# Performance work log

Measured on AMD Instinct MI355X. Metric: run time of the kernel, lower is better.

The kernel has to match this reference:

```python
import jax, jax.numpy as jnp
import numpy as np

B, H, L, N, F = 32, 256, 2048, 64, 32  # batch, d_model, seq len, d_state//2 complex modes, num_features


def setup_inputs() -> dict:
    key = jax.random.key(0)
    ks = jax.random.split(key, 16)
    inp = {
        "x": jax.random.normal(ks[0], (B, H, L), jnp.float32),
        "t": jax.random.normal(ks[1], (B, H), jnp.float32),
        "features": jax.random.normal(ks[2], (B, F, L), jnp.float32),
        # time_linear
        "Wt": jax.random.normal(ks[3], (H, H), jnp.float32) / np.sqrt(H),
        "bt": jnp.zeros((H,), jnp.float32),
        # LayerNorm over d_model
        "ln_g": jnp.ones((H,), jnp.float32),
        "ln_b": jnp.zeros((H,), jnp.float32),
        # S4 (diagonal / S4D parameterization, d_state=128 -> N=64 complex, bidirectional)
        "log_dt": jnp.log(jnp.full((H,), 0.01, jnp.float32))
                  + jax.random.uniform(ks[4], (H,), jnp.float32, -1.0, 1.0),
        "logA_real": jnp.log(0.5 * jnp.ones((H, N), jnp.float32)),
        "A_imag": jnp.broadcast_to(np.pi * jnp.arange(N, dtype=jnp.float32), (H, N)).copy(),
        "C_re": jax.random.normal(ks[5], (2, H, N), jnp.float32) / np.sqrt(2 * N),
        "C_im": jax.random.normal(ks[6], (2, H, N), jnp.float32) / np.sqrt(2 * N),
        "D": jax.random.normal(ks[7], (H,), jnp.float32),
        # S4 output position-wise linear
        "Wout": jax.random.normal(ks[8], (H, H), jnp.float32) / np.sqrt(H),
        "bout": jnp.zeros((H,), jnp.float32),
        # out_linear1 / out_linear2 (1x1 convs)
        "W1": jax.random.normal(ks[9], (H, H), jnp.float32) / np.sqrt(H),
        "b1": jnp.zeros((H,), jnp.float32),
        "W2": jax.random.normal(ks[10], (H, H), jnp.float32) / np.sqrt(H),
        "b2": jnp.zeros((H,), jnp.float32),
        # feature_encoder 1x1 conv
        "Wf": jax.random.normal(ks[11], (H, F), jnp.float32) / np.sqrt(F),
        "bf": jnp.zeros((H,), jnp.float32),
    }
    return inp


def _s4_block(x, t, features, Wt, bt, ln_g, ln_b, log_dt, logA_real, A_imag,
              C_re, C_im, D, Wout, bout, W1, b1, W2, b2, Wf, bf):
    Bb, Hh, Ll = x.shape
    # time conditioning: Linear(t) broadcast over length  -> (B,H,L)
    tb = t @ Wt.T + bt
    xin = x + tb[:, :, None]
    # LayerNorm over channel (d_model) axis (norm applied on transposed tensor)
    mu = jnp.mean(xin, axis=1, keepdims=True)
    var = jnp.var(xin, axis=1, keepdims=True)
    z = (xin - mu) / jnp.sqrt(var + 1e-5) * ln_g[None, :, None] + ln_b[None, :, None]
    # --- bidirectional S4 (diagonal SSM) kernel ---
    dt = jnp.exp(log_dt)                       # (H,)
    A = -jnp.exp(logA_real) + 1j * A_imag      # (H,N)
    dtA = dt[:, None] * A                      # (H,N)
    Cd = (C_re + 1j * C_im) * (jnp.exp(dtA) - 1.0) / A      # (2,H,N) discretized C
    vand = jnp.exp(dtA[:, :, None] * jnp.arange(Ll))         # (H,N,L) Vandermonde
    K = 2.0 * jnp.real(jnp.einsum('chn,hnl->chl', Cd, vand))  # (2,H,L)
    zeros = jnp.zeros_like(K[0])
    k = jnp.concatenate([K[0], zeros], -1) + jnp.concatenate([zeros, K[1][:, ::-1]], -1)  # (H,2L)
    # FFT global convolution
    y = jnp.fft.irfft(jnp.fft.rfft(z, 2 * Ll) * jnp.fft.rfft(k, 2 * Ll)[None], 2 * Ll)[..., :Ll]
    y = y + z * D[None, :, None]
    y = jax.nn.gelu(y)
    y = jnp.einsum('bhl,gh->bgl', y, Wout) + bout[None, :, None]
    xr = y + xin                                # residual inside S4Layer
    # feature encoder + gated activation
    out = xr + jnp.einsum('bfl,hf->bhl', features, Wf) + bf[None, :, None]
    g = jnp.tanh(out) * jax.nn.sigmoid(out)
    o1 = jnp.einsum('bhl,gh->bgl', g, W1) + b1[None, :, None]
    o2 = jnp.einsum('bhl,gh->bgl', g, W2) + b2[None, :, None]
    return (o1 + x, o2)


def reference(x, t, features, Wt, bt, ln_g, ln_b, log_dt, logA_real, A_imag,
              C_re, C_im, D, Wout, bout, W1, b1, W2, b2, Wf, bf):
    return _s4_block(x, t, features, Wt, bt, ln_g, ln_b, log_dt, logA_real, A_imag,
                     C_re, C_im, D, Wout, bout, W1, b1, W2, b2, Wf, bf)
```

## Files before the change

### kernel.cpp

```cpp
#include <hip/hip_runtime.h>

typedef unsigned short ushort_t;

#define Bb 32
#define Hh 256
#define Ll 2048
#define Nn 64
#define BHL 16777216

typedef __bf16 bf16x8 __attribute__((ext_vector_type(8)));
typedef float f32x4 __attribute__((ext_vector_type(4)));
typedef unsigned int uint4v __attribute__((ext_vector_type(4)));

__device__ __forceinline__ ushort_t f2bf(float f) {
    unsigned int u = __float_as_uint(f);
    unsigned int r = ((u >> 16) & 1u) + 0x7fffu;
    return (ushort_t)((u + r) >> 16);
}
__device__ __forceinline__ float bf2f(ushort_t h) {
    return __uint_as_float(((unsigned int)h) << 16);
}
__device__ __forceinline__ float gelu_tanh(float v) {
    float u = 0.7978845608028654f * fmaf(0.044715f * v, v * v, v);
    float e = __expf(2.f * u);
    float th = 1.f - 2.f / (e + 1.f);
    return 0.5f * v * (1.f + th);
}
__device__ __forceinline__ float gate_fn(float v) {
    float sg = 1.f / (1.f + __expf(-v));
    float e2 = __expf(2.f * v);
    float th = 1.f - 2.f / (e2 + 1.f);
    return th * sg;
}
__device__ __forceinline__ uint4v rev8v(uint4v a) {
    union { uint4v v; ushort_t s8[8]; } x, y;
    x.v = a;
    #pragma unroll
    for (int j = 0; j < 8; ++j) y.s8[j] = x.s8[7 - j];
    return y.v;
}

__global__ __launch_bounds__(256) void prep_kernel(
    const float* __restrict__ t, const float* __restrict__ Wt, const float* __restrict__ bt,
    const float* __restrict__ Wout, const float* __restrict__ Wf,
    const float* __restrict__ bout, const float* __restrict__ bfb,
    const float* __restrict__ W1, const float* __restrict__ b1,
    const float* __restrict__ W2, const float* __restrict__ b2,
    float* __restrict__ tb, float* __restrict__ bc, float* __restrict__ b12,
    ushort_t* __restrict__ wcf, ushort_t* __restrict__ w12f)
{
    int bx = blockIdx.x, tid = threadIdx.x;
    __shared__ float trow[256];
    if (bx < 32) {
        trow[tid] = t[bx * 256 + tid];
        __syncthreads();
        float acc = bt[tid];
        #pragma unroll 4
        for (int hh = 0; hh < 256; ++hh) acc = fmaf(trow[hh], Wt[tid * 256 + hh], acc);
        tb[bx * 256 + tid] = acc;
    } else if (bx < 64) {
        int gt = (bx - 32) * 256 + tid;
        if (gt < 256) bc[gt] = bout[gt] + bfb[gt];
        if (gt < 512) b12[gt] = (gt < 256) ? b1[gt] : b2[gt - 256];
        for (int fg = gt; fg < 9216; fg += 8192) {
            int mt = fg / 576, rem = fg % 576;
            int kc = rem >> 6, lane = rem & 63;
            int m = mt * 16 + (lane & 15);
            int kb = kc * 32 + (lane >> 4) * 8;
            #pragma unroll
            for (int j = 0; j < 8; ++j) {
                int k = kb + j;
                float v = (k < 256) ? Wout[m * 256 + k] : Wf[m * 32 + (k - 256)];
                wcf[(size_t)fg * 8 + j] = f2bf(v);
            }
        }
    } else {
        int gt = (bx - 64) * 256 + tid;
        for (int fg = gt; fg < 16384; fg += 8192) {
            int mt = fg >> 9, rem = fg & 511;
            int kc = rem >> 6, lane = rem & 63;
            int m = mt * 16 + (lane & 15);
            int kb = kc * 32 + (lane >> 4) * 8;
            #pragma unroll
            for (int j = 0; j < 8; ++j) {
                int k = kb + j;
                float v = (m < 256) ? W1[m * 256 + k] : W2[(m - 256) * 256 + k];
                w12f[(size_t)fg * 8 + j] = f2bf(v);
            }
        }
    }
}

__global__ __launch_bounds__(256) void prep2_kernel(
    const float* __restrict__ log_dt, const float* __restrict__ logA, const float* __restrict__ Aimg,
    const float* __restrict__ C_re, const float* __restrict__ C_im,
    float* __restrict__ drg, float* __restrict__ dig,
    ushort_t* __restrict__ Mfrag, ushort_t* __restrict__ Vfrag)
{
    int bx = blockIdx.x, tid = threadIdx.x;
    int h = bx >> 1, dir = bx & 1;
    __shared__ float drL[64], diL[64], crL[64], ciL[64];
    __shared__ float ktab[128];
    __shared__ ushort_t bndL[128 * 128];
    if (tid < 64) {
        int n = tid;
        int idx = h * 64 + n;
        float dt = __expf(log_dt[h]);
        float Ar = -__expf(logA[idx]);
        float Ai = Aimg[idx];
        float dr = dt * Ar, di = dt * Ai;
        float er = __expf(dr);
        float wr_ = er * __cosf(di), wi_ = er * __sinf(di);
        float nr = wr_ - 1.f, ni = wi_;
        float inv = 1.f / (Ar * Ar + Ai * Ai);
        float qr = (nr * Ar + ni * Ai) * inv;
        float qi = (ni * Ar - nr * Ai) * inv;
        float cr = C_re[dir * 16384 + idx], ci = C_im[dir * 16384 + idx];
        drL[n] = dr; diL[n] = di;
        crL[n] = 2.f * (cr * qr - ci * qi);
        ciL[n] = 2.f * (cr * qi + ci * qr);
        if (dir == 0) { drg[idx] = dr; dig[idx] = di; }
    }
    __syncthreads();
    if (tid < 128) {
        int i = tid;
        float e = (float)(i + 1 - dir);
        #pragma unroll 4
        for (int n = 0; n < 64; ++n) {
            float ex = __expf(e * drL[n]);
            float ph = e * diL[n];
            float pr = ex * __cosf(ph), pi = ex * __sinf(ph);
            bndL[i * 128 + n]      = f2bf(crL[n] * pr - ciL[n] * pi);
            bndL[i * 128 + 64 + n] = f2bf(-(crL[n] * pi + ciL[n] * pr));
        }
    } else {
        int d = tid - 128;
        float e = (float)d;
        float acc = 0.f;
        #pragma unroll 4
        for (int n = 0; n < 64; ++n) {
            float ex = __expf(e * drL[n]);
            float ph = e * diL[n];
            acc += crL[n] * (ex * __cosf(ph)) - ciL[n] * (ex * __sinf(ph));
        }
        ktab[d] = acc;
    }
    __syncthreads();
    size_t base = (size_t)bx << 15;
    for (int idx = tid; idx < 32768; idx += 256) {
        int j = idx & 7, lane = (idx >> 3) & 63, kc = (idx >> 9) & 7, mt = idx >> 12;
        int m = mt * 16 + (lane & 15);
        int k = kc * 32 + (lane >> 4) * 8 + j;
        float v;
        if (k < 128) {
            int d = m - k - dir;
            v = (d >= 0) ? ktab[d] : 0.f;
        } else {
            v = bf2f(bndL[m * 128 + (k - 128)]);
        }
        Mfrag[base + idx] = f2bf(v);
    }
    if (dir == 0) {
        size_t vbase = (size_t)h << 14;
        for (int idx = tid; idx < 16384; idx += 256) {
            int j = idx & 7, lane = (idx >> 3) & 63, kc = (idx >> 9) & 3, mt = idx >> 11;
            int s = mt * 16 + (lane & 15);
            int k = kc * 32 + (lane >> 4) * 8 + j;
            int n = s & 63;
            float e = (float)(127 - k);
            float ex = __expf(e * drL[n]);
            float ph = e * diL[n];
            float v = (s < 64) ? ex * __cosf(ph) : ex * __sinf(ph);
            Vfrag[vbase + idx] = f2bf(v);
        }
    }
}

__global__ __launch_bounds__(256) void ln_kernel(
    const float* __restrict__ x, const float* __restrict__ tb,
    const float* __restrict__ ln_g, const float* __restrict__ ln_b,
    ushort_t* __restrict__ zbf)
{
    int gid = blockIdx.x * 256 + threadIdx.x;
    int b = gid >> 11, l = gid & 2047;
    const float* xp = x + (size_t)b * (Hh * Ll) + l;
    const float* tbp = tb + b * 256;
    float sum = 0.f, ssq = 0.f;
    #pragma unroll 8
    for (int h = 0; h < 256; ++h) {
        float v = xp[(size_t)h * Ll] + tbp[h];
        sum += v; ssq = fmaf(v, v, ssq);
    }
    float mean = sum * (1.f / 256.f);
    float var = fmaf(ssq, 1.f / 256.f, -mean * mean);
    float rstd = rsqrtf(var + 1e-5f);
    ushort_t* zp = zbf + (size_t)b * (Hh * Ll) + l;
    #pragma unroll 8
    for (int h = 0; h < 256; ++h) {
        float v = xp[(size_t)h * Ll] + tbp[h];
        zp[(size_t)h * Ll] = f2bf((v - mean) * rstd * ln_g[h] + ln_b[h]);
    }
}

__global__ __launch_bounds__(256) void ssm_mega_kernel(
    const ushort_t* __restrict__ zbf,
    const float* __restrict__ drg, const float* __restrict__ dig, const float* __restrict__ Dv,
    const ushort_t* __restrict__ Mfrag, const ushort_t* __restrict__ Vfrag,
    ushort_t* __restrict__ ya)
{
    __shared__ ushort_t Zs[64 * 136];
    __shared__ ushort_t Ssf[64 * 136];
    __shared__ ushort_t Ssb[64 * 136];
    __shared__ float Qb[2 * 128 * 17];
    int tid = threadIdx.x, lane = tid & 63, w = tid >> 6;
    int q = lane >> 4, cl = lane & 15;
    int h = blockIdx.x, cb = blockIdx.y;
    int b0 = cb * 4;
    for (int i = tid; i < 1024; i += 256) {
        int bsub = i >> 8, t8 = (i & 255) * 8;
        const ushort_t* zrow = zbf + ((size_t)((b0 + bsub) * 256 + h) << 11);
        *(uint4v*)&Zs[(bsub * 16 + (t8 >> 7)) * 136 + (t8 & 127)] = *(const uint4v*)(zrow + t8);
    }
    float dr0 = drg[h * 64 + lane], di0 = dig[h * 64 + lane];
    float ex128 = __expf(128.f * dr0);
    float w128r = ex128 * __cosf(128.f * di0);
    float w128i = ex128 * __sinf(128.f * di0);
    float Dh = Dv[h];
    __syncthreads();
    const ushort_t* vbase = Vfrag + ((size_t)h << 14);
    const ushort_t* mbase0 = Mfrag + ((size_t)(h * 2) << 15);
    const ushort_t* mbase1 = Mfrag + ((size_t)(h * 2 + 1) << 15);
    for (int bsub = 0; bsub < 4; ++bsub) {
        f32x4 qa[2][2] = {};
        #pragma unroll
        for (int kc = 0; kc < 4; ++kc) {
            int kk = kc * 32 + q * 8;
            bf16x8 bz = __builtin_bit_cast(bf16x8,
                *(const uint4v*)&Zs[(bsub * 16 + cl) * 136 + kk]);
            bf16x8 bzr = __builtin_bit_cast(bf16x8, rev8v(
                *(const uint4v*)&Zs[(bsub * 16 + (15 - cl)) * 136 + (120 - kk)]));
            #pragma unroll
            for (int i = 0; i < 2; ++i) {
                int mt = w * 2 + i;
                bf16x8 af = __builtin_bit_cast(bf16x8,
                    *(const uint4v*)(vbase + (((mt * 4 + kc) * 64 + lane) << 3)));
                qa[0][i] = __builtin_amdgcn_mfma_f32_16x16x32_bf16(af, bz, qa[0][i], 0, 0, 0);
                qa[1][i] = __builtin_amdgcn_mfma_f32_16x16x32_bf16(af, bzr, qa[1][i], 0, 0, 0);
            }
        }
        __syncthreads();
        #pragma unroll
        for (int d = 0; d < 2; ++d)
            #pragma unroll
            for (int i = 0; i < 2; ++i) {
                int mt = w * 2 + i;
                #pragma unroll
                for (int r = 0; r < 4; ++r)
                    Qb[d * 2176 + (mt * 16 + q * 4 + r) * 17 + cl] = qa[d][i][r];
            }
        __syncthreads();
        if (w < 2) {
            ushort_t* S = (w == 0) ? Ssf : Ssb;
            const float* Qp = Qb + w * 2176;
            float sre = 0.f, sim = 0.f;
            for (int cc = 0; cc < 16; ++cc) {
                S[(bsub * 16 + cc) * 136 + lane] = f2bf(sre);
                S[(bsub * 16 + cc) * 136 + 64 + lane] = f2bf(sim);
                float qre = Qp[lane * 17 + cc];
                float qim = Qp[(64 + lane) * 17 + cc];
                float nre = fmaf(w128r, sre, fmaf(-w128i, sim, qre));
                float nim = fmaf(w128r, sim, fmaf(w128i, sre, qim));
                sre = nre; sim = nim;
            }
        }
        __syncthreads();
    }
    f32x4 accf[2][4] = {}, accb[2][4] = {};
    for (int kc = 0; kc < 8; ++kc) {
        int kk = (kc & 3) * 32 + q * 8;
        bf16x8 aff[2], afb[2];
        #pragma unroll
        for (int i = 0; i < 2; ++i) {
            int mt = w * 2 + i;
            aff[i] = __builtin_bit_cast(bf16x8, *(const uint4v*)(mbase0 + (((mt * 8 + kc) * 64 + lane) << 3)));
            afb[i] = __builtin_bit_cast(bf16x8, *(const uint4v*)(mbase1 + (((mt * 8 + kc) * 64 + lane) << 3)));
        }
        #pragma unroll
        for (int nt = 0; nt < 4; ++nt) {
            bf16x8 bff, bfb_;
            if (kc < 4) {
                bff  = __builtin_bit_cast(bf16x8, *(const uint4v*)&Zs[(nt * 16 + cl) * 136 + kk]);
                bfb_ = __builtin_bit_cast(bf16x8, rev8v(
                       *(const uint4v*)&Zs[(nt * 16 + (15 - cl)) * 136 + (120 - kk)]));
            } else {
                bff  = __builtin_bit_cast(bf16x8, *(const uint4v*)&Ssf[(nt * 16 + cl) * 136 + kk]);
                bfb_ = __builtin_bit_cast(bf16x8, *(const uint4v*)&Ssb[(nt * 16 + cl) * 136 + kk]);
            }
            #pragma unroll
            for (int i = 0; i < 2; ++i) {
                accf[i][nt] = __builtin_amdgcn_mfma_f32_16x16x32_bf16(aff[i], bff,  accf[i][nt], 0, 0, 0);
                accb[i][nt] = __builtin_amdgcn_mfma_f32_16x16x32_bf16(afb[i], bfb_, accb[i][nt], 0, 0, 0);
            }
        }
    }
    __syncthreads();
    ushort_t* Yf = Ssf;
    ushort_t* Yb = Ssb;
    #pragma unroll
    for (int i = 0; i < 2; ++i) {
        int mt = w * 2 + i;
        #pragma unroll
        for (int nt = 0; nt < 4; ++nt) {
            int col = nt * 16 + cl;
            #pragma unroll
            for (int r = 0; r < 4; ++r) {
                int m = mt * 16 + q * 4 + r;
                Yf[col * 136 + m] = f2bf(accf[i][nt][r]);
                Yb[col * 136 + m] = f2bf(accb[i][nt][r]);
            }
        }
    }
    __syncthreads();
    for (int u = tid; u < 1024; u += 256) {
        int col = u >> 4, i0 = (u & 15) * 8;
        int bsub = col >> 4, c = col & 15;
        int colb = bsub * 16 + (15 - c);
        union { uint4v v; ushort_t s8[8]; } uf, uz, ub, uo;
        uf.v = *(const uint4v*)&Yf[col * 136 + i0];
        uz.v = *(const uint4v*)&Zs[col * 136 + i0];
        ub.v = rev8v(*(const uint4v*)&Yb[colb * 136 + (120 - i0)]);
        #pragma unroll
        for (int j = 0; j < 8; ++j) {
            float v = bf2f(uf.s8[j]) + bf2f(ub.s8[j]) + Dh * bf2f(uz.s8[j]);
            uo.s8[j] = f2bf(gelu_tanh(v));
        }
        ushort_t* yrow = ya + ((size_t)((b0 + bsub) * 256 + h) << 11);
        *(uint4v*)(yrow + c * 128 + i0) = uo.v;
    }
}

__global__ __launch_bounds__(256, 4) void gemm1_kernel(
    const ushort_t* __restrict__ ya, const float* __restrict__ feat,
    const float* __restrict__ x, const float* __restrict__ tb,
    const float* __restrict__ bc, const ushort_t* __restrict__ wcf,
    ushort_t* __restrict__ g)
{
    __shared__ __align__(16) ushort_t XT[64 * 48];
    int tid = threadIdx.x;
    int w = tid >> 6, lane = tid & 63;
    int bx = blockIdx.x;
    int b = bx >> 5;
    int l0 = (bx & 31) << 6;
    f32x4 acc[4][4] = {};
    int kk = tid >> 3, ng = tid & 7;
    for (int kc = 0; kc < 9; ++kc) {
        int k = kc * 32 + kk;
        union { uint4v v; ushort_t s[8]; } u;
        if (k < 256) {
            u.v = *(const uint4v*)(ya + ((size_t)(b * 256 + k) << 11) + l0 + ng * 8);
        } else {
            const float* src = feat + (size_t)(b * 32 + (k - 256)) * Ll + l0 + ng * 8;
            #pragma unroll
            for (int j = 0; j < 8; ++j) u.s[j] = f2bf(src[j]);
        }
        #pragma unroll
        for (int j = 0; j < 8; ++j) XT[(ng * 8 + j) * 48 + kk] = u.s[j];
        __syncthreads();
        bf16x8 af[4], bfr[4];
        #pragma unroll
        for (int i = 0; i < 4; ++i) {
            const ushort_t* p = wcf + ((size_t)((w * 4 + i) * 9 + kc) * 64 + lane) * 8;
            af[i] = __builtin_bit_cast(bf16x8, *(const uint4v*)p);
        }
        #pragma unroll
        for (int nt = 0; nt < 4; ++nt) {
            const ushort_t* p = &XT[(nt * 16 + (lane & 15)) * 48 + (lane >> 4) * 8];
            bfr[nt] = __builtin_bit_cast(bf16x8, *(const uint4v*)p);
        }
        #pragma unroll
        for (int i = 0; i < 4; ++i)
            #pragma unroll
            for (int nt = 0; nt < 4; ++nt)
                acc[i][nt] = __builtin_amdgcn_mfma_f32_16x16x32_bf16(af[i], bfr[nt], acc[i][nt], 0, 0, 0);
        __syncthreads();
    }
    int q = lane >> 4, nl = lane & 15;
    #pragma unroll
    for (int i = 0; i < 4; ++i) {
        #pragma unroll
        for (int nt = 0; nt < 4; ++nt) {
            int n = l0 + nt * 16 + nl;
            #pragma unroll
            for (int r = 0; r < 4; ++r) {
                int m = (w * 4 + i) * 16 + q * 4 + r;
                size_t oi = (size_t)(b * 256 + m) * Ll + n;
                float v = acc[i][nt][r] + bc[m] + tb[b * 256 + m] + x[oi];
                g[oi] = f2bf(gate_fn(v));
            }
        }
    }
}

__global__ __launch_bounds__(256, 4) void gemm2_kernel(
    const ushort_t* __restrict__ g, const float* __restrict__ x,
    const float* __restrict__ b12, const ushort_t* __restrict__ w12f,
    float* __restrict__ out)
{
    __shared__ __align__(16) ushort_t XT[64 * 48];
    int tid = threadIdx.x;
    int w = tid >> 6, lane = tid & 63;
    int bx = blockIdx.x;
    int half = blockIdx.y;
    int b = bx >> 5;
    int l0 = (bx & 31) << 6;
    f32x4 acc[4][4] = {};
    int kk = tid >> 3, ng = tid & 7;
    for (int kc = 0; kc < 8; ++kc) {
        int k = kc * 32 + kk;
        union { uint4v v; ushort_t s[8]; } u;
        u.v = *(const uint4v*)(g + (size_t)(b * 256 + k) * Ll + l0 + ng * 8);
        #pragma unroll
        for (int j = 0; j < 8; ++j) XT[(ng * 8 + j) * 48 + kk] = u.s[j];
        __syncthreads();
        bf16x8 af[4], bfr[4];
        #pragma unroll
        for (int i = 0; i < 4; ++i) {
            int mtg = half * 16 + w * 4 + i;
            const ushort_t* p = w12f + ((size_t)(mtg * 8 + kc) * 64 + lane) * 8;
            af[i] = __builtin_bit_cast(bf16x8, *(const uint4v*)p);
        }
        #pragma unroll
        for (int nt = 0; nt < 4; ++nt) {
            const ushort_t* p = &XT[(nt * 16 + (lane & 15)) * 48 + (lane >> 4) * 8];
            bfr[nt] = __builtin_bit_cast(bf16x8, *(const uint4v*)p);
        }
        #pragma unroll
        for (int i = 0; i < 4; ++i)
            #pragma unroll
            for (int nt = 0; nt < 4; ++nt)
                acc[i][nt] = __builtin_amdgcn_mfma_f32_16x16x32_bf16(af[i], bfr[nt], acc[i][nt], 0, 0, 0);
        __syncthreads();
    }
    int q = lane >> 4, nl = lane & 15;
    #pragma unroll
    for (int i = 0; i < 4; ++i) {
        #pragma unroll
        for (int nt = 0; nt < 4; ++nt) {
            int n = l0 + nt * 16 + nl;
            #pragma unroll
            for (int r = 0; r < 4; ++r) {
                int m = (w * 4 + i) * 16 + q * 4 + r;
                size_t oi = (size_t)(b * 256 + m) * Ll + n;
                float v = acc[i][nt][r] + b12[half * 256 + m];
                if (half == 0) out[oi] = v + x[oi];
                else out[(size_t)BHL + oi] = v;
            }
        }
    }
}

extern "C" void kernel_launch(void* const* d_in, const int* in_sizes, int n_in,
                              void* d_out, int out_size, void* d_ws, size_t ws_size,
                              hipStream_t stream) {
    const float* x      = (const float*)d_in[0];
    const float* t      = (const float*)d_in[1];
    const float* feat   = (const float*)d_in[2];
    const float* Wt     = (const float*)d_in[3];
    const float* bt     = (const float*)d_in[4];
    const float* ln_g   = (const float*)d_in[5];
    const float* ln_b   = (const float*)d_in[6];
    const float* log_dt = (const float*)d_in[7];
    const float* logA   = (const float*)d_in[8];
    const float* Aimg   = (const float*)d_in[9];
    const float* C_re   = (const float*)d_in[10];
    const float* C_im   = (const float*)d_in[11];
    const float* Dv     = (const float*)d_in[12];
    const float* Wout   = (const float*)d_in[13];
    const float* bout   = (const float*)d_in[14];
    const float* W1     = (const float*)d_in[15];
    const float* b1     = (const float*)d_in[16];
    const float* W2     = (const float*)d_in[17];
    const float* b2     = (const float*)d_in[18];
    const float* Wf     = (const float*)d_in[19];
    const float* bfb    = (const float*)d_in[20];

    char* ob = (char*)d_out;
    ushort_t* zbf = (ushort_t*)ob;
    ushort_t* yab = (ushort_t*)(ob + 33554432);
    float*    out = (float*)d_out;

    char* ws = (char*)d_ws;
    ushort_t* Mfrag = (ushort_t*)ws;
    ushort_t* gbuf  = (ushort_t*)ws;
    ushort_t* Vfrag = (ushort_t*)(ws + 33554432);
    char* ws2 = ws + 33554432 + 8388608;
    float* tb   = (float*)ws2;
    float* drg  = (float*)(ws2 + 32768);
    float* dig  = (float*)(ws2 + 98304);
    float* bc   = (float*)(ws2 + 163840);
    float* b12  = (float*)(ws2 + 164864);
    ushort_t* wcf  = (ushort_t*)(ws2 + 166912);
    ushort_t* w12f = (ushort_t*)(ws2 + 314368);

    prep_kernel<<<96, 256, 0, stream>>>(t, Wt, bt, Wout, Wf, bout, bfb, W1, b1, W2, b2,
                                        tb, bc, b12, wcf, w12f);
    prep2_kernel<<<512, 256, 0, stream>>>(log_dt, logA, Aimg, C_re, C_im, drg, dig, Mfrag, Vfrag);
    ln_kernel<<<256, 256, 0, stream>>>(x, tb, ln_g, ln_b, zbf);
    ssm_mega_kernel<<<dim3(256, 8), 256, 0, stream>>>(zbf, drg, dig, Dv, Mfrag, Vfrag, yab);
    gemm1_kernel<<<1024, 256, 0, stream>>>(yab, feat, x, tb, bc, wcf, gbuf);
    gemm2_kernel<<<dim3(1024, 2), 256, 0, stream>>>(gbuf, x, b12, w12f, out);
}
```

Measured before the change: 428.5 us.

## Fuse gate GEMMs via LDS, merge prep kernels, tile LayerNorm through shared memory

The two output GEMMs become one kernel: the gated activation is written to an LDS tile and fed straight into the W1/W2 GEMM, so the bf16 intermediate no longer goes through global memory and there is one launch fewer. The two prep kernels are merged into a single launch. LayerNorm now stages a 256x64 slab of x in LDS with float4 loads and writes with 8-byte stores, instead of reading x twice with strided per-thread access. The fused GEMM holds twice as many accumulators and uses about 34KB of extra LDS, lowering occupancy, and the SSM output buffer moves from the output region into the workspace.

```diff
diff --git a/kernel.cpp b/kernel.cpp
--- a/kernel.cpp
+++ b/kernel.cpp
@@ -11,6 +11,7 @@
 typedef __bf16 bf16x8 __attribute__((ext_vector_type(8)));
 typedef float f32x4 __attribute__((ext_vector_type(4)));
 typedef unsigned int uint4v __attribute__((ext_vector_type(4)));
+typedef unsigned int uint2v __attribute__((ext_vector_type(2)));
 
 __device__ __forceinline__ ushort_t f2bf(float f) {
     unsigned int u = __float_as_uint(f);
@@ -40,17 +41,24 @@
     return y.v;
 }
 
-__global__ __launch_bounds__(256) void prep_kernel(
+__global__ __launch_bounds__(256) void prep_all_kernel(
     const float* __restrict__ t, const float* __restrict__ Wt, const float* __restrict__ bt,
     const float* __restrict__ Wout, const float* __restrict__ Wf,
     const float* __restrict__ bout, const float* __restrict__ bfb,
     const float* __restrict__ W1, const float* __restrict__ b1,
     const float* __restrict__ W2, const float* __restrict__ b2,
+    const float* __restrict__ log_dt, const float* __restrict__ logA, const float* __restrict__ Aimg,
+    const float* __restrict__ C_re, const float* __restrict__ C_im,
     float* __restrict__ tb, float* __restrict__ bc, float* __restrict__ b12,
-    ushort_t* __restrict__ wcf, ushort_t* __restrict__ w12f)
+    ushort_t* __restrict__ wcf, ushort_t* __restrict__ w12f,
+    float* __restrict__ drg, float* __restrict__ dig,
+    ushort_t* __restrict__ Mfrag, ushort_t* __restrict__ Vfrag)
 {
     int bx = blockIdx.x, tid = threadIdx.x;
     __shared__ float trow[256];
+    __shared__ float drL[64], diL[64], crL[64], ciL[64];
+    __shared__ float ktab[128];
+    __shared__ ushort_t bndL[128 * 128];
     if (bx < 32) {
         trow[tid] = t[bx * 256 + tid];
         __syncthreads();
@@ -58,7 +66,9 @@
         #pragma unroll 4
         for (int hh = 0; hh < 256; ++hh) acc = fmaf(trow[hh], Wt[tid * 256 + hh], acc);
         tb[bx * 256 + tid] = acc;
-    } else if (bx < 64) {
+        return;
+    }
+    if (bx < 64) {
         int gt = (bx - 32) * 256 + tid;
         if (gt < 256) bc[gt] = bout[gt] + bfb[gt];
         if (gt < 512) b12[gt] = (gt < 256) ? b1[gt] : b2[gt - 256];
@@ -74,7 +84,9 @@
                 wcf[(size_t)fg * 8 + j] = f2bf(v);
             }
         }
-    } else {
+        return;
+    }
+    if (bx < 96) {
         int gt = (bx - 64) * 256 + tid;
         for (int fg = gt; fg < 16384; fg += 8192) {
             int mt = fg >> 9, rem = fg & 511;
@@ -88,20 +100,10 @@
                 w12f[(size_t)fg * 8 + j] = f2bf(v);
             }
         }
-    }
-}
-
-__global__ __launch_bounds__(256) void prep2_kernel(
-    const float* __restrict__ log_dt, const float* __restrict__ logA, const float* __restrict__ Aimg,
-    const float* __restrict__ C_re, const float* __restrict__ C_im,
-    float* __restrict__ drg, float* __restrict__ dig,
-    ushort_t* __restrict__ Mfrag, ushort_t* __restrict__ Vfrag)
-{
-    int bx = blockIdx.x, tid = threadIdx.x;
-    int h = bx >> 1, dir = bx & 1;
-    __shared__ float drL[64], diL[64], crL[64], ciL[64];
-    __shared__ float ktab[128];
-    __shared__ ushort_t bndL[128 * 128];
+        return;
+    }
+    int bx2 = bx - 96;
+    int h = bx2 >> 1, dir = bx2 & 1;
     if (tid < 64) {
         int n = tid;
         int idx = h * 64 + n;
@@ -146,7 +148,7 @@
         ktab[d] = acc;
     }
     __syncthreads();
-    size_t base = (size_t)bx << 15;
+    size_t base = (size_t)bx2 << 15;
     for (int idx = tid; idx < 32768; idx += 256) {
         int j = idx & 7, lane = (idx >> 3) & 63, kc = (idx >> 9) & 7, mt = idx >> 12;
         int m = mt * 16 + (lane & 15);
@@ -176,29 +178,58 @@
     }
 }
 
-__global__ __launch_bounds__(256) void ln_kernel(
+__global__ __launch_bounds__(256) void ln1_kernel(
     const float* __restrict__ x, const float* __restrict__ tb,
     const float* __restrict__ ln_g, const float* __restrict__ ln_b,
     ushort_t* __restrict__ zbf)
 {
-    int gid = blockIdx.x * 256 + threadIdx.x;
-    int b = gid >> 11, l = gid & 2047;
-    const float* xp = x + (size_t)b * (Hh * Ll) + l;
-    const float* tbp = tb + b * 256;
+    __shared__ float xs[256 * 64];
+    __shared__ float tbg[256], lng[256], lnb[256];
+    __shared__ float red[2 * 256];
+    __shared__ float murs[2 * 64];
+    int tid = threadIdx.x;
+    int b = blockIdx.x >> 5, l0 = (blockIdx.x & 31) << 6;
+    tbg[tid] = tb[b * 256 + tid];
+    lng[tid] = ln_g[tid];
+    lnb[tid] = ln_b[tid];
+    const float* xb = x + ((size_t)b * 256) * 2048 + l0;
+    for (int i = tid; i < 4096; i += 256) {
+        int h = i >> 4, c4 = (i & 15) * 4;
+        *(float4*)&xs[h * 64 + c4] = *(const float4*)(xb + (size_t)h * 2048 + c4);
+    }
+    __syncthreads();
+    int c = tid & 63, w = tid >> 6;
     float sum = 0.f, ssq = 0.f;
     #pragma unroll 8
-    for (int h = 0; h < 256; ++h) {
-        float v = xp[(size_t)h * Ll] + tbp[h];
+    for (int hh = 0; hh < 64; ++hh) {
+        int h = w * 64 + hh;
+        float v = xs[h * 64 + c] + tbg[h];
         sum += v; ssq = fmaf(v, v, ssq);
     }
-    float mean = sum * (1.f / 256.f);
-    float var = fmaf(ssq, 1.f / 256.f, -mean * mean);
-    float rstd = rsqrtf(var + 1e-5f);
-    ushort_t* zp = zbf + (size_t)b * (Hh * Ll) + l;
-    #pragma unroll 8
-    for (int h = 0; h < 256; ++h) {
-        float v = xp[(size_t)h * Ll] + tbp[h];
-        zp[(size_t)h * Ll] = f2bf((v - mean) * rstd * ln_g[h] + ln_b[h]);
+    red[w * 64 + c] = sum;
+    red[256 + w * 64 + c] = ssq;
+    __syncthreads();
+    if (tid < 64) {
+        float s = red[tid] + red[64 + tid] + red[128 + tid] + red[192 + tid];
+        float q = red[256 + tid] + red[320 + tid] + red[384 + tid] + red[448 + tid];
+        float mean = s * (1.f / 256.f);
+        float var = fmaf(q, 1.f / 256.f, -mean * mean);
+        murs[tid] = mean;
+        murs[64 + tid] = rsqrtf(var + 1e-5f);
+    }
+    __syncthreads();
+    ushort_t* zb = zbf + ((size_t)b * 256) * 2048 + l0;
+    for (int i = tid; i < 4096; i += 256) {
+        int h = i >> 4, c4 = (i & 15) * 4;
+        float g = lng[h], be = lnb[h], tbh = tbg[h];
+        union { unsigned long long u; ushort_t s4[4]; } o;
+        #pragma unroll
+        for (int j = 0; j < 4; ++j) {
+            int cc = c4 + j;
+            float v = xs[h * 64 + cc] + tbh;
+            o.s4[j] = f2bf((v - murs[cc]) * murs[64 + cc] * g + be);
+        }
+        *(unsigned long long*)(zb + (size_t)h * 2048 + c4) = o.u;
     }
 }
 
@@ -339,19 +370,22 @@
     }
 }
 
-__global__ __launch_bounds__(256, 4) void gemm1_kernel(
+__global__ __launch_bounds__(256, 2) void gemm12_kernel(
     const ushort_t* __restrict__ ya, const float* __restrict__ feat,
     const float* __restrict__ x, const float* __restrict__ tb,
-    const float* __restrict__ bc, const ushort_t* __restrict__ wcf,
-    ushort_t* __restrict__ g)
+    const float* __restrict__ bc, const float* __restrict__ b12,
+    const ushort_t* __restrict__ wcf, const ushort_t* __restrict__ w12f,
+    float* __restrict__ out)
 {
     __shared__ __align__(16) ushort_t XT[64 * 48];
+    __shared__ __align__(16) ushort_t GT[64 * 264];
     int tid = threadIdx.x;
     int w = tid >> 6, lane = tid & 63;
-    int bx = blockIdx.x;
-    int b = bx >> 5;
-    int l0 = (bx & 31) << 6;
-    f32x4 acc[4][4] = {};
+    int q = lane >> 4, nl = lane & 15;
+    int b = blockIdx.x >> 5;
+    int l0 = (blockIdx.x & 31) << 6;
+    const float* xb = x + ((size_t)b * 256) * 2048 + l0;
+    f32x4 acc1[4][4] = {};
     int kk = tid >> 3, ng = tid & 7;
     for (int kc = 0; kc < 9; ++kc) {
         int k = kc * 32 + kk;
@@ -359,7 +393,7 @@
         if (k < 256) {
             u.v = *(const uint4v*)(ya + ((size_t)(b * 256 + k) << 11) + l0 + ng * 8);
         } else {
-            const float* src = feat + (size_t)(b * 32 + (k - 256)) * Ll + l0 + ng * 8;
+            const float* src = feat + (size_t)(b * 32 + (k - 256)) * 2048 + l0 + ng * 8;
             #pragma unroll
             for (int j = 0; j < 8; ++j) u.s[j] = f2bf(src[j]);
         }
@@ -374,86 +408,66 @@
         }
         #pragma unroll
         for (int nt = 0; nt < 4; ++nt) {
-            const ushort_t* p = &XT[(nt * 16 + (lane & 15)) * 48 + (lane >> 4) * 8];
+            const ushort_t* p = &XT[(nt * 16 + nl) * 48 + q * 8];
             bfr[nt] = __builtin_bit_cast(bf16x8, *(const uint4v*)p);
         }
         #pragma unroll
         for (int i = 0; i < 4; ++i)
             #pragma unroll
             for (int nt = 0; nt < 4; ++nt)
-                acc[i][nt] = __builtin_amdgcn_mfma_f32_16x16x32_bf16(af[i], bfr[nt], acc[i][nt], 0, 0, 0);
+                acc1[i][nt] = __builtin_amdgcn_mfma_f32_16x16x32_bf16(af[i], bfr[nt], acc1[i][nt], 0, 0, 0);
         __syncthreads();
     }
-    int q = lane >> 4, nl = lane & 15;
     #pragma unroll
     for (int i = 0; i < 4; ++i) {
         #pragma unroll
         for (int nt = 0; nt < 4; ++nt) {
-            int n = l0 + nt * 16 + nl;
+            int c = nt * 16 + nl;
             #pragma unroll
             for (int r = 0; r < 4; ++r) {
                 int m = (w * 4 + i) * 16 + q * 4 + r;
-                size_t oi = (size_t)(b * 256 + m) * Ll + n;
-                float v = acc[i][nt][r] + bc[m] + tb[b * 256 + m] + x[oi];
-                g[oi] = f2bf(gate_fn(v));
-            }
-        }
-    }
-}
-
-__global__ __launch_bounds__(256, 4) void gemm2_kernel(
-    const ushort_t* __restrict__ g, const float* __restrict__ x,
-    const float* __restrict__ b12, const ushort_t* __restrict__ w12f,
-    float* __restrict__ out)
-{
-    __shared__ __align__(16) ushort_t XT[64 * 48];
-    int tid = threadIdx.x;
-    int w = tid >> 6, lane = tid & 63;
-    int bx = blockIdx.x;
-    int half = blockIdx.y;
-    int b = bx >> 5;
-    int l0 = (bx & 31) << 6;
-    f32x4 acc[4][4] = {};
-    int kk = tid >> 3, ng = tid & 7;
+                float v = acc1[i][nt][r] + bc[m] + tb[b * 256 + m] + xb[(size_t)m * 2048 + c];
+                GT[c * 264 + m] = f2bf(gate_fn(v));
+            }
+        }
+    }
+    __syncthreads();
+    f32x4 acc2[8][4] = {};
     for (int kc = 0; kc < 8; ++kc) {
-        int k = kc * 32 + kk;
-        union { uint4v v; ushort_t s[8]; } u;
-        u.v = *(const uint4v*)(g + (size_t)(b * 256 + k) * Ll + l0 + ng * 8);
-        #pragma unroll
-        for (int j = 0; j < 8; ++j) XT[(ng * 8 + j) * 48 + kk] = u.s[j];
-        __syncthreads();
-        bf16x8 af[4], bfr[4];
-        #pragma unroll
-        for (int i = 0; i < 4; ++i) {
-            int mtg = half * 16 + w * 4 + i;
-            const ushort_t* p = w12f + ((size_t)(mtg * 8 + kc) * 64 + lane) * 8;
+        bf16x8 af[8], bfr[4];
+        #pragma unroll
+        for (int i = 0; i < 8; ++i) {
+            int mt = w * 8 + i;
+            const ushort_t* p = w12f + ((size_t)(mt * 8 + kc) * 64 + lane) * 8;
             af[i] = __builtin_bit_cast(bf16x8, *(const uint4v*)p);
         }
         #pragma unroll
         for (int nt = 0; nt < 4; ++nt) {
-            const ushort_t* p = &XT[(nt * 16 + (lane & 15)) * 48 + (lane >> 4) * 8];
+            const ushort_t* p = &GT[(nt * 16 + nl) * 264 + kc * 32 + q * 8];
             bfr[nt] = __builtin_bit_cast(bf16x8, *(const uint4v*)p);
         }
         #pragma unroll
-        for (int i = 0; i < 4; ++i)
+        for (int i = 0; i < 8; ++i)
             #pragma unroll
             for (int nt = 0; nt < 4; ++nt)
-                acc[i][nt] = __builtin_amdgcn_mfma_f32_16x16x32_bf16(af[i], bfr[nt], acc[i][nt], 0, 0, 0);
-        __syncthreads();
-    }
-    int q = lane >> 4, nl = lane & 15;
+                acc2[i][nt] = __builtin_amdgcn_mfma_f32_16x16x32_bf16(af[i], bfr[nt], acc2[i][nt], 0, 0, 0);
+    }
     #pragma unroll
-    for (int i = 0; i < 4; ++i) {
+    for (int i = 0; i < 8; ++i) {
+        int mt = w * 8 + i;
         #pragma unroll
         for (int nt = 0; nt < 4; ++nt) {
             int n = l0 + nt * 16 + nl;
+            int c = nt * 16 + nl;
             #pragma unroll
             for (int r = 0; r < 4; ++r) {
-                int m = (w * 4 + i) * 16 + q * 4 + r;
-                size_t oi = (size_t)(b * 256 + m) * Ll + n;
-                float v = acc[i][nt][r] + b12[half * 256 + m];
-                if (half == 0) out[oi] = v + x[oi];
-                else out[(size_t)BHL + oi] = v;
+                int m2 = mt * 16 + q * 4 + r;
+                float v = acc2[i][nt][r] + b12[m2];
+                if (m2 < 256) {
+                    out[(size_t)(b * 256 + m2) * 2048 + n] = v + xb[(size_t)m2 * 2048 + c];
+                } else {
+                    out[(size_t)BHL + (size_t)(b * 256 + (m2 - 256)) * 2048 + n] = v;
+                }
             }
         }
     }
@@ -486,14 +500,13 @@
 
     char* ob = (char*)d_out;
     ushort_t* zbf = (ushort_t*)ob;
-    ushort_t* yab = (ushort_t*)(ob + 33554432);
     float*    out = (float*)d_out;
 
     char* ws = (char*)d_ws;
     ushort_t* Mfrag = (ushort_t*)ws;
-    ushort_t* gbuf  = (ushort_t*)ws;
     ushort_t* Vfrag = (ushort_t*)(ws + 33554432);
-    char* ws2 = ws + 33554432 + 8388608;
+    ushort_t* yab   = (ushort_t*)(ws + 41943040);
+    char* ws2 = ws + 75497472;
     float* tb   = (float*)ws2;
     float* drg  = (float*)(ws2 + 32768);
     float* dig  = (float*)(ws2 + 98304);
@@ -502,11 +515,10 @@
     ushort_t* wcf  = (ushort_t*)(ws2 + 166912);
     ushort_t* w12f = (ushort_t*)(ws2 + 314368);
 
-    prep_kernel<<<96, 256, 0, stream>>>(t, Wt, bt, Wout, Wf, bout, bfb, W1, b1, W2, b2,
-                                        tb, bc, b12, wcf, w12f);
-    prep2_kernel<<<512, 256, 0, stream>>>(log_dt, logA, Aimg, C_re, C_im, drg, dig, Mfrag, Vfrag);
-    ln_kernel<<<256, 256, 0, stream>>>(x, tb, ln_g, ln_b, zbf);
+    prep_all_kernel<<<608, 256, 0, stream>>>(t, Wt, bt, Wout, Wf, bout, bfb, W1, b1, W2, b2,
+                                             log_dt, logA, Aimg, C_re, C_im,
+                                             tb, bc, b12, wcf, w12f, drg, dig, Mfrag, Vfrag);
+    ln1_kernel<<<1024, 256, 0, stream>>>(x, tb, ln_g, ln_b, zbf);
     ssm_mega_kernel<<<dim3(256, 8), 256, 0, stream>>>(zbf, drg, dig, Dv, Mfrag, Vfrag, yab);
-    gemm1_kernel<<<1024, 256, 0, stream>>>(yab, feat, x, tb, bc, wcf, gbuf);
-    gemm2_kernel<<<dim3(1024, 2), 256, 0, stream>>>(gbuf, x, b12, w12f, out);
-}
+    gemm12_kernel<<<1024, 256, 0, stream>>>(yab, feat, x, tb, bc, b12, wcf, w12f, out);
+}
```

After: 446.5 us. 1.04x slower.
